# Kernel optimization log

Measured on AMD Instinct MI355X. Metric: run time of the kernel, lower is better.

The kernel has to match this reference:

```python
import jax, jax.numpy as jnp
import numpy as np

H = 8  # hidden_size


def lstm_layer(x, w_ih, w_hh, b_ih, b_hh):
    """Single LSTM layer, seq-first x: [T, B, in] -> hidden seq [T, B, H].
    PyTorch gate order: i, f, g, o."""
    # Precompute input contribution for all timesteps (one big GEMM).
    zx = jnp.einsum('tbi,gi->tbg', x, w_ih) + b_ih + b_hh  # [T, B, 4H]
    B = x.shape[1]
    h0 = jnp.zeros((B, H), x.dtype)
    c0 = jnp.zeros((B, H), x.dtype)

    def step(carry, zx_t):
        h, c = carry
        z = zx_t + h @ w_hh.T  # [B, 4H]
        i = jax.nn.sigmoid(z[:, 0 * H:1 * H])
        f = jax.nn.sigmoid(z[:, 1 * H:2 * H])
        g = jnp.tanh(z[:, 2 * H:3 * H])
        o = jax.nn.sigmoid(z[:, 3 * H:4 * H])
        c_new = f * c + i * g
        h_new = o * jnp.tanh(c_new)
        return (h_new, c_new), h_new

    _, hs = jax.lax.scan(step, (h0, c0), zx)
    return hs  # [T, B, H]


def setup_inputs() -> dict:
    key = jax.random.key(0)
    ks = jax.random.split(key, 12)
    T, B, IN, OUT = 1024, 16384, 2, 1
    k = 1.0 / np.sqrt(H)  # torch default init bound

    def unif(kk, shape):
        return jax.random.uniform(kk, shape, jnp.float32, -k, k)

    x = jax.random.normal(ks[0], (T, B, IN), jnp.float32)
    return {
        'x': x,
        'w_ih_l0': unif(ks[1], (4 * H, IN)),
        'w_hh_l0': unif(ks[2], (4 * H, H)),
        'b_ih_l0': unif(ks[3], (4 * H,)),
        'b_hh_l0': unif(ks[4], (4 * H,)),
        'w_ih_l1': unif(ks[5], (4 * H, H)),
        'w_hh_l1': unif(ks[6], (4 * H, H)),
        'b_ih_l1': unif(ks[7], (4 * H,)),
        'b_hh_l1': unif(ks[8], (4 * H,)),
        'fc_w': unif(ks[9], (OUT, H)),
        'fc_b': unif(ks[10], (OUT,)),
    }


def reference(x, w_ih_l0, w_hh_l0, b_ih_l0, b_hh_l0,
              w_ih_l1, w_hh_l1, b_ih_l1, b_hh_l1, fc_w, fc_b):
    h = lstm_layer(x, w_ih_l0, w_hh_l0, b_ih_l0, b_hh_l0)   # layer 0
    h = lstm_layer(h, w_ih_l1, w_hh_l1, b_ih_l1, b_hh_l1)   # layer 1
    last = h[-1]                                            # [B, H]
    return last @ fc_w.T + fc_b                             # [B, out]
```

## Files before the change

### kernel.cpp

```cpp
#include <hip/hip_runtime.h>

#define TSTEPS 1024
#define BATCH 16384

template<int K>
__device__ __forceinline__ float bc8(float v) {
    return __int_as_float(__builtin_amdgcn_ds_swizzle(__float_as_int(v), (K << 5) | 0x18));
}
__device__ __forceinline__ void gather8(float* d, float v) {
    d[0] = bc8<0>(v); d[1] = bc8<1>(v); d[2] = bc8<2>(v); d[3] = bc8<3>(v);
    d[4] = bc8<4>(v); d[5] = bc8<5>(v); d[6] = bc8<6>(v); d[7] = bc8<7>(v);
}

__device__ __forceinline__ float sig_s(float zs) {
    return __builtin_amdgcn_rcpf(1.0f + __builtin_amdgcn_exp2f(zs));
}
__device__ __forceinline__ float tanh_s(float zs) {
    return __builtin_fmaf(2.0f, __builtin_amdgcn_rcpf(1.0f + __builtin_amdgcn_exp2f(zs)), -1.0f);
}
__device__ __forceinline__ float tanh_raw(float c) {
    return tanh_s(c * -2.88539008f);
}

__global__ __launch_bounds__(256, 2) void lstm2_fused(
    const float* __restrict__ x,
    const float* __restrict__ w_ih_l0, const float* __restrict__ w_hh_l0,
    const float* __restrict__ b_ih_l0, const float* __restrict__ b_hh_l0,
    const float* __restrict__ w_ih_l1, const float* __restrict__ w_hh_l1,
    const float* __restrict__ b_ih_l1, const float* __restrict__ b_hh_l1,
    const float* __restrict__ fc_w, const float* __restrict__ fc_b,
    float* __restrict__ out)
{
    const int tid = blockIdx.x * blockDim.x + threadIdx.x;
    const int j = tid & 7;
    const int b = tid >> 3;

    const float sc[4] = {-1.44269504f, -1.44269504f, -2.88539008f, -1.44269504f};

    float wi0x[4], wi0y[4], wh0[4][8], zb0[4];
    float wi1[4][8], wh1[4][8], zb1[4];
#pragma unroll
    for (int g = 0; g < 4; ++g) {
        const int r = g * 8 + j;
        const float s = sc[g];
        wi0x[g] = s * w_ih_l0[r * 2 + 0];
        wi0y[g] = s * w_ih_l0[r * 2 + 1];
        zb0[g]  = s * (b_ih_l0[r] + b_hh_l0[r]);
        zb1[g]  = s * (b_ih_l1[r] + b_hh_l1[r]);
#pragma unroll
        for (int k = 0; k < 8; ++k) {
            wh0[g][k] = s * w_hh_l0[r * 8 + k];
            wi1[g][k] = s * w_ih_l1[r * 8 + k];
            wh1[g][k] = s * w_hh_l1[r * 8 + k];
        }
    }
    const float fcw = fc_w[j];
    const float fcb = fc_b[0];

    float h0 = 0.f, c0 = 0.f, h1 = 0.f, c1 = 0.f;
    float h0v[8], h1v[8];
#pragma unroll
    for (int k = 0; k < 8; ++k) { h0v[k] = 0.f; h1v[k] = 0.f; }

    const float2* xp = reinterpret_cast<const float2*>(x) + b;
    float2 xv = xp[0];
    float2 xn = xp[BATCH];

    for (int t = 0; t < TSTEPS; ++t) {
        float2 xn2 = (t + 2 < TSTEPS) ? xp[2 * BATCH] : xv;
        xp += BATCH;

        float z0[4], z1[4];
#pragma unroll
        for (int g = 0; g < 4; ++g) {
            z0[g] = __builtin_fmaf(wi0y[g], xv.y, __builtin_fmaf(wi0x[g], xv.x, zb0[g]));
            z1[g] = zb1[g];
#pragma unroll
            for (int k = 0; k < 8; ++k) {
                z0[g] = __builtin_fmaf(wh0[g][k], h0v[k], z0[g]);
                z1[g] = __builtin_fmaf(wh1[g][k], h1v[k], z1[g]);
            }
        }
        const float gi = sig_s(z0[0]), gf = sig_s(z0[1]);
        const float gg = tanh_s(z0[2]), go = sig_s(z0[3]);
        c0 = __builtin_fmaf(gf, c0, gi * gg);
        h0 = go * tanh_raw(c0);

        gather8(h0v, h0);
#pragma unroll
        for (int g = 0; g < 4; ++g) {
#pragma unroll
            for (int k = 0; k < 8; ++k)
                z1[g] = __builtin_fmaf(wi1[g][k], h0v[k], z1[g]);
        }
        const float i1 = sig_s(z1[0]), f1 = sig_s(z1[1]);
        const float g1 = tanh_s(z1[2]), o1 = sig_s(z1[3]);
        c1 = __builtin_fmaf(f1, c1, i1 * g1);
        h1 = o1 * tanh_raw(c1);

        gather8(h1v, h1);

        xv = xn; xn = xn2;
    }

    float p = fcw * h1;
    p += __shfl_xor(p, 1);
    p += __shfl_xor(p, 2);
    p += __shfl_xor(p, 4);
    if (j == 0) out[b] = p + fcb;
}

extern "C" void kernel_launch(void* const* d_in, const int* in_sizes, int n_in,
                              void* d_out, int out_size, void* d_ws, size_t ws_size,
                              hipStream_t stream) {
    const float* x       = (const float*)d_in[0];
    const float* w_ih_l0 = (const float*)d_in[1];
    const float* w_hh_l0 = (const float*)d_in[2];
    const float* b_ih_l0 = (const float*)d_in[3];
    const float* b_hh_l0 = (const float*)d_in[4];
    const float* w_ih_l1 = (const float*)d_in[5];
    const float* w_hh_l1 = (const float*)d_in[6];
    const float* b_ih_l1 = (const float*)d_in[7];
    const float* b_hh_l1 = (const float*)d_in[8];
    const float* fc_w    = (const float*)d_in[9];
    const float* fc_b    = (const float*)d_in[10];
    float* out = (float*)d_out;

    const int threads = 256;
    const int blocks  = (BATCH * 8) / threads;
    lstm2_fused<<<blocks, threads, 0, stream>>>(
        x, w_ih_l0, w_hh_l0, b_ih_l0, b_hh_l0,
        w_ih_l1, w_hh_l1, b_ih_l1, b_hh_l1, fc_w, fc_b, out);
}
```

Baseline: 934.7 us.

## Use 4 lanes per batch row with packed FMA and DPP quad rotations

Each batch element is now handled by 4 lanes instead of 8, with each lane owning two hidden units packed into a float2 so the recurrent matvecs can use packed FP32 FMA. The 8-way ds_swizzle broadcast is replaced by three DPP quad-rotations per state, and weights are pre-permuted to match the rotated order. Accumulation is split into two partial chains to shorten dependency latency. This halves the thread count and doubles per-thread register use (launch bounds lowered to 1), trading occupancy for less cross-lane traffic and more arithmetic per instruction.

```diff
diff --git a/kernel.cpp b/kernel.cpp
--- a/kernel.cpp
+++ b/kernel.cpp
@@ -3,14 +3,25 @@
 #define TSTEPS 1024
 #define BATCH 16384
 
-template<int K>
-__device__ __forceinline__ float bc8(float v) {
-    return __int_as_float(__builtin_amdgcn_ds_swizzle(__float_as_int(v), (K << 5) | 0x18));
+typedef float f32x2 __attribute__((ext_vector_type(2)));
+
+template<int R>
+__device__ __forceinline__ float qrot(float v) {
+    constexpr int ctrl = ((R) & 3) | ((((R) + 1) & 3) << 2) |
+                         ((((R) + 2) & 3) << 4) | ((((R) + 3) & 3) << 6);
+    return __int_as_float(__builtin_amdgcn_mov_dpp(__float_as_int(v), ctrl, 0xF, 0xF, false));
 }
-__device__ __forceinline__ void gather8(float* d, float v) {
-    d[0] = bc8<0>(v); d[1] = bc8<1>(v); d[2] = bc8<2>(v); d[3] = bc8<3>(v);
-    d[4] = bc8<4>(v); d[5] = bc8<5>(v); d[6] = bc8<6>(v); d[7] = bc8<7>(v);
+template<int R>
+__device__ __forceinline__ f32x2 qrot2(f32x2 v) {
+    f32x2 r; r.x = qrot<R>(v.x); r.y = qrot<R>(v.y); return r;
 }
+
+__device__ __forceinline__ f32x2 fma2(f32x2 a, f32x2 b, f32x2 c) {
+    return __builtin_elementwise_fma(a, b, c);
+}
+__device__ __forceinline__ f32x2 splat2(float v) { f32x2 r; r.x = v; r.y = v; return r; }
+__device__ __forceinline__ f32x2 splx(f32x2 p) { return splat2(p.x); }
+__device__ __forceinline__ f32x2 sply(f32x2 p) { return splat2(p.y); }
 
 __device__ __forceinline__ float sig_s(float zs) {
     return __builtin_amdgcn_rcpf(1.0f + __builtin_amdgcn_exp2f(zs));
@@ -18,11 +29,11 @@
 __device__ __forceinline__ float tanh_s(float zs) {
     return __builtin_fmaf(2.0f, __builtin_amdgcn_rcpf(1.0f + __builtin_amdgcn_exp2f(zs)), -1.0f);
 }
-__device__ __forceinline__ float tanh_raw(float c) {
-    return tanh_s(c * -2.88539008f);
-}
+__device__ __forceinline__ f32x2 sig2(f32x2 z)    { f32x2 r; r.x = sig_s(z.x);  r.y = sig_s(z.y);  return r; }
+__device__ __forceinline__ f32x2 tanh2_s(f32x2 z) { f32x2 r; r.x = tanh_s(z.x); r.y = tanh_s(z.y); return r; }
+__device__ __forceinline__ f32x2 tanh2_raw(f32x2 c) { return tanh2_s(c * splat2(-2.88539008f)); }
 
-__global__ __launch_bounds__(256, 2) void lstm2_fused(
+__global__ __launch_bounds__(256, 1) void lstm2_fused(
     const float* __restrict__ x,
     const float* __restrict__ w_ih_l0, const float* __restrict__ w_hh_l0,
     const float* __restrict__ b_ih_l0, const float* __restrict__ b_hh_l0,
@@ -32,35 +43,49 @@
     float* __restrict__ out)
 {
     const int tid = blockIdx.x * blockDim.x + threadIdx.x;
-    const int j = tid & 7;
-    const int b = tid >> 3;
+    const int q   = tid & 3;
+    const int b   = tid >> 2;
 
     const float sc[4] = {-1.44269504f, -1.44269504f, -2.88539008f, -1.44269504f};
 
-    float wi0x[4], wi0y[4], wh0[4][8], zb0[4];
-    float wi1[4][8], wh1[4][8], zb1[4];
+    f32x2 wx[4][2], zb0[4], zb1[4];
+    f32x2 wh0[4][4][2], wi1[4][4][2], wh1[4][4][2];
 #pragma unroll
     for (int g = 0; g < 4; ++g) {
-        const int r = g * 8 + j;
+        const int ra = g * 8 + q, rb = g * 8 + q + 4;
         const float s = sc[g];
-        wi0x[g] = s * w_ih_l0[r * 2 + 0];
-        wi0y[g] = s * w_ih_l0[r * 2 + 1];
-        zb0[g]  = s * (b_ih_l0[r] + b_hh_l0[r]);
-        zb1[g]  = s * (b_ih_l1[r] + b_hh_l1[r]);
+        wx[g][0].x = s * w_ih_l0[ra * 2 + 0]; wx[g][0].y = s * w_ih_l0[rb * 2 + 0];
+        wx[g][1].x = s * w_ih_l0[ra * 2 + 1]; wx[g][1].y = s * w_ih_l0[rb * 2 + 1];
+        zb0[g].x = s * (b_ih_l0[ra] + b_hh_l0[ra]); zb0[g].y = s * (b_ih_l0[rb] + b_hh_l0[rb]);
+        zb1[g].x = s * (b_ih_l1[ra] + b_hh_l1[ra]); zb1[g].y = s * (b_ih_l1[rb] + b_hh_l1[rb]);
 #pragma unroll
-        for (int k = 0; k < 8; ++k) {
-            wh0[g][k] = s * w_hh_l0[r * 8 + k];
-            wi1[g][k] = s * w_ih_l1[r * 8 + k];
-            wh1[g][k] = s * w_hh_l1[r * 8 + k];
+        for (int r = 0; r < 4; ++r) {
+            const int sl = (q + r) & 3;
+            wh0[g][r][0].x = s * w_hh_l0[ra * 8 + sl];     wh0[g][r][0].y = s * w_hh_l0[rb * 8 + sl];
+            wh0[g][r][1].x = s * w_hh_l0[ra * 8 + sl + 4]; wh0[g][r][1].y = s * w_hh_l0[rb * 8 + sl + 4];
+            wi1[g][r][0].x = s * w_ih_l1[ra * 8 + sl];     wi1[g][r][0].y = s * w_ih_l1[rb * 8 + sl];
+            wi1[g][r][1].x = s * w_ih_l1[ra * 8 + sl + 4]; wi1[g][r][1].y = s * w_ih_l1[rb * 8 + sl + 4];
+            wh1[g][r][0].x = s * w_hh_l1[ra * 8 + sl];     wh1[g][r][0].y = s * w_hh_l1[rb * 8 + sl];
+            wh1[g][r][1].x = s * w_hh_l1[ra * 8 + sl + 4]; wh1[g][r][1].y = s * w_hh_l1[rb * 8 + sl + 4];
         }
     }
-    const float fcw = fc_w[j];
+#pragma unroll
+    for (int g = 0; g < 4; ++g) {
+        asm volatile("" : "+v"(wx[g][0]), "+v"(wx[g][1]), "+v"(zb0[g]), "+v"(zb1[g]));
+#pragma unroll
+        for (int r = 0; r < 4; ++r)
+            asm volatile("" : "+v"(wh0[g][r][0]), "+v"(wh0[g][r][1]),
+                             "+v"(wi1[g][r][0]), "+v"(wi1[g][r][1]),
+                             "+v"(wh1[g][r][0]), "+v"(wh1[g][r][1]));
+    }
+
+    f32x2 fcw; fcw.x = fc_w[q]; fcw.y = fc_w[q + 4];
     const float fcb = fc_b[0];
 
-    float h0 = 0.f, c0 = 0.f, h1 = 0.f, c1 = 0.f;
-    float h0v[8], h1v[8];
+    f32x2 h0p = splat2(0.f), c0p = splat2(0.f), h1p = splat2(0.f), c1p = splat2(0.f);
+    f32x2 R0[4], R1[4];
 #pragma unroll
-    for (int k = 0; k < 8; ++k) { h0v[k] = 0.f; h1v[k] = 0.f; }
+    for (int r = 0; r < 4; ++r) { R0[r] = splat2(0.f); R1[r] = splat2(0.f); }
 
     const float2* xp = reinterpret_cast<const float2*>(x) + b;
     float2 xv = xp[0];
@@ -70,44 +95,63 @@
         float2 xn2 = (t + 2 < TSTEPS) ? xp[2 * BATCH] : xv;
         xp += BATCH;
 
-        float z0[4], z1[4];
+        f32x2 za[4], zbq[4];
 #pragma unroll
         for (int g = 0; g < 4; ++g) {
-            z0[g] = __builtin_fmaf(wi0y[g], xv.y, __builtin_fmaf(wi0x[g], xv.x, zb0[g]));
-            z1[g] = zb1[g];
-#pragma unroll
-            for (int k = 0; k < 8; ++k) {
-                z0[g] = __builtin_fmaf(wh0[g][k], h0v[k], z0[g]);
-                z1[g] = __builtin_fmaf(wh1[g][k], h1v[k], z1[g]);
-            }
+            za[g] = fma2(wx[g][1], splat2(xv.y), fma2(wx[g][0], splat2(xv.x), zb0[g]));
+            za[g] = fma2(wh0[g][0][0], splx(R0[0]), za[g]);
+            za[g] = fma2(wh0[g][0][1], sply(R0[0]), za[g]);
+            za[g] = fma2(wh0[g][1][0], splx(R0[1]), za[g]);
+            za[g] = fma2(wh0[g][1][1], sply(R0[1]), za[g]);
+            zbq[g] =      wh0[g][2][0] * splx(R0[2]);
+            zbq[g] = fma2(wh0[g][2][1], sply(R0[2]), zbq[g]);
+            zbq[g] = fma2(wh0[g][3][0], splx(R0[3]), zbq[g]);
+            zbq[g] = fma2(wh0[g][3][1], sply(R0[3]), zbq[g]);
         }
-        const float gi = sig_s(z0[0]), gf = sig_s(z0[1]);
-        const float gg = tanh_s(z0[2]), go = sig_s(z0[3]);
-        c0 = __builtin_fmaf(gf, c0, gi * gg);
-        h0 = go * tanh_raw(c0);
-
-        gather8(h0v, h0);
+        f32x2 ya[4], yb[4];
 #pragma unroll
         for (int g = 0; g < 4; ++g) {
+            ya[g] = fma2(wh1[g][0][0], splx(R1[0]), zb1[g]);
+            ya[g] = fma2(wh1[g][0][1], sply(R1[0]), ya[g]);
+            ya[g] = fma2(wh1[g][1][0], splx(R1[1]), ya[g]);
+            ya[g] = fma2(wh1[g][1][1], sply(R1[1]), ya[g]);
+            yb[g] =      wh1[g][2][0] * splx(R1[2]);
+            yb[g] = fma2(wh1[g][2][1], sply(R1[2]), yb[g]);
+            yb[g] = fma2(wh1[g][3][0], splx(R1[3]), yb[g]);
+            yb[g] = fma2(wh1[g][3][1], sply(R1[3]), yb[g]);
+        }
+        f32x2 z0i = za[0] + zbq[0], z0f = za[1] + zbq[1];
+        f32x2 z0g = za[2] + zbq[2], z0o = za[3] + zbq[3];
+        c0p = fma2(sig2(z0f), c0p, sig2(z0i) * tanh2_s(z0g));
+        h0p = sig2(z0o) * tanh2_raw(c0p);
+
+        R0[0] = h0p; R0[1] = qrot2<1>(h0p); R0[2] = qrot2<2>(h0p); R0[3] = qrot2<3>(h0p);
+
 #pragma unroll
-            for (int k = 0; k < 8; ++k)
-                z1[g] = __builtin_fmaf(wi1[g][k], h0v[k], z1[g]);
+        for (int g = 0; g < 4; ++g) {
+            f32x2 pa, pb;
+            pa =      wi1[g][0][0] * splx(R0[0]);
+            pa = fma2(wi1[g][0][1], sply(R0[0]), pa);
+            pa = fma2(wi1[g][1][0], splx(R0[1]), pa);
+            pa = fma2(wi1[g][1][1], sply(R0[1]), pa);
+            pb =      wi1[g][2][0] * splx(R0[2]);
+            pb = fma2(wi1[g][2][1], sply(R0[2]), pb);
+            pb = fma2(wi1[g][3][0], splx(R0[3]), pb);
+            pb = fma2(wi1[g][3][1], sply(R0[3]), pb);
+            ya[g] = (ya[g] + yb[g]) + (pa + pb);
         }
-        const float i1 = sig_s(z1[0]), f1 = sig_s(z1[1]);
-        const float g1 = tanh_s(z1[2]), o1 = sig_s(z1[3]);
-        c1 = __builtin_fmaf(f1, c1, i1 * g1);
-        h1 = o1 * tanh_raw(c1);
+        c1p = fma2(sig2(ya[1]), c1p, sig2(ya[0]) * tanh2_s(ya[2]));
+        h1p = sig2(ya[3]) * tanh2_raw(c1p);
 
-        gather8(h1v, h1);
+        R1[0] = h1p; R1[1] = qrot2<1>(h1p); R1[2] = qrot2<2>(h1p); R1[3] = qrot2<3>(h1p);
 
         xv = xn; xn = xn2;
     }
 
-    float p = fcw * h1;
+    float p = __builtin_fmaf(fcw.y, h1p.y, fcw.x * h1p.x);
     p += __shfl_xor(p, 1);
     p += __shfl_xor(p, 2);
-    p += __shfl_xor(p, 4);
-    if (j == 0) out[b] = p + fcb;
+    if ((tid & 3) == 0) out[b] = p + fcb;
 }
 
 extern "C" void kernel_launch(void* const* d_in, const int* in_sizes, int n_in,
@@ -127,7 +171,7 @@
     float* out = (float*)d_out;
 
     const int threads = 256;
-    const int blocks  = (BATCH * 8) / threads;
+    const int blocks  = (BATCH * 4) / threads;
     lstm2_fused<<<blocks, threads, 0, stream>>>(
         x, w_ih_l0, w_hh_l0, b_ih_l0, b_hh_l0,
         w_ih_l1, w_hh_l1, b_ih_l1, b_hh_l1, fc_w, fc_b, out);
```

Measured after the change: 1.070 ms. 14.5% more time.
